# Kernel tuning notes

Hardware: AMD Instinct MI355X
Metric: run time of the kernel (lower is better)

Reference implementation:

```python
import jax, jax.numpy as jnp
import numpy as np

B, H, W, C = 4, 192, 640, 32
S = 32
STEPS = np.arange(S, dtype=np.float32)  # depth steps (init kwarg 'steps')


def setup_inputs() -> dict:
    key = jax.random.key(0)
    k1, k2, k3, k4, k5 = jax.random.split(key, 5)
    x = jax.random.normal(k1, (B, H, W, C), jnp.float32)
    y = jax.random.normal(k2, (B, H, W, C), jnp.float32)
    # principal point near image center, focal ~500px, small translation T12
    origin = jnp.array([[W / 2.0, H / 2.0]], jnp.float32) + jax.random.uniform(k3, (B, 2), jnp.float32)
    focal = 500.0 + 50.0 * jax.random.uniform(k4, (B, 2), jnp.float32)
    T12 = 0.01 * jax.random.normal(k5, (B, 3), jnp.float32)
    return {"x": x, "y": y, "origin": origin, "focal": focal, "T12": T12}


def _bilinear_1img(img, sx, sy):
    # img [H,W,C]; sx [W]: source x-coord for each output column; sy [H]: source y per row.
    # Matches tf.contrib.image.transform BILINEAR with fill value 0 outside the image.
    x0 = jnp.floor(sx); fx = sx - x0
    y0 = jnp.floor(sy); fy = sy - y0
    x0i = x0.astype(jnp.int32); x1i = x0i + 1
    y0i = y0.astype(jnp.int32); y1i = y0i + 1
    mx0 = ((x0i >= 0) & (x0i < W)).astype(img.dtype)
    mx1 = ((x1i >= 0) & (x1i < W)).astype(img.dtype)
    my0 = ((y0i >= 0) & (y0i < H)).astype(img.dtype)
    my1 = ((y1i >= 0) & (y1i < H)).astype(img.dtype)
    # interpolate along y first (transform is separable: x'=a*x+b, y'=a*y+c)
    r0 = img[jnp.clip(y0i, 0, H - 1)]                     # [H,W,C]
    r1 = img[jnp.clip(y1i, 0, H - 1)]                     # [H,W,C]
    rows = (my0 * (1.0 - fy))[:, None, None] * r0 + (my1 * fy)[:, None, None] * r1
    c0 = rows[:, jnp.clip(x0i, 0, W - 1)]                 # [H,W,C]
    c1 = rows[:, jnp.clip(x1i, 0, W - 1)]
    return (mx0 * (1.0 - fx))[None, :, None] * c0 + (mx1 * fx)[None, :, None] * c1


_warp = jax.vmap(lambda img, a, b, c: _bilinear_1img(
    img,
    a * jnp.arange(W, dtype=img.dtype) + b,
    a * jnp.arange(H, dtype=img.dtype) + c))


def reference(x, y, origin, focal, T12):
    tz = T12[:, 2]  # [B]

    def per_step(d):
        safe_d = jnp.where(d == 0.0, 1.0, d)
        D = jnp.where(d == 0.0, 0.0, 1.0 / (1.0 / safe_d + tz))          # [B]
        alpha = 1.0 - D * tz                                              # [B]
        beta = D * tz * origin[:, 0] + D * focal[:, 0] * T12[:, 0]        # [B]
        gamma = D * tz * origin[:, 1] + D * focal[:, 1] * T12[:, 1]       # [B]
        shifted = _warp(x, alpha, beta, gamma)                            # [B,H,W,C]
        return jnp.mean(shifted * y, axis=3)                              # [B,H,W]

    corr = jax.lax.map(jax.checkpoint(per_step), jnp.asarray(STEPS))      # [S,B,H,W]
    return jnp.transpose(corr, (1, 2, 3, 0))                              # [B,H,W,S]
```

## Files before the change

### kernel.cpp

```cpp
#include <hip/hip_runtime.h>
#include <hip/hip_fp16.h>

#define BB 4
#define HH 192
#define WW 640
#define CC 32
#define SS 32
#define PXB 64
#define SPH 8

typedef _Float16 half2n __attribute__((ext_vector_type(2)));

#if defined(__has_builtin)
#if __has_builtin(__builtin_amdgcn_fdot2)
#define HAS_FDOT2 1
#endif
#endif

__global__ __launch_bounds__(256) void convert_x_kernel(const float* __restrict__ x,
                                                        __half* __restrict__ xh) {
    const size_t i = ((size_t)blockIdx.x * 256 + threadIdx.x) * 8;
    const float4 f0 = *(const float4*)(x + i);
    const float4 f1 = *(const float4*)(x + i + 4);
    uint4 u;
    u.x = __builtin_bit_cast(unsigned, __floats2half2_rn(f0.x, f0.y));
    u.y = __builtin_bit_cast(unsigned, __floats2half2_rn(f0.z, f0.w));
    u.z = __builtin_bit_cast(unsigned, __floats2half2_rn(f1.x, f1.y));
    u.w = __builtin_bit_cast(unsigned, __floats2half2_rn(f1.z, f1.w));
    *(uint4*)(xh + i) = u;
}

__global__ __launch_bounds__(256, 7) void corr_kernel(
    const __half* __restrict__ xh, const float* __restrict__ y,
    const float* __restrict__ origin, const float* __restrict__ focal,
    const float* __restrict__ T12, float* __restrict__ out)
{
    __shared__ uint4 sOff[SPH * PXB];
    __shared__ uint4 sWt [SPH * PXB];

    const int tid  = threadIdx.x;
    const int lane = tid & 63;
    const int wave = tid >> 6;
    const int slot = lane >> 2;
    const int cg   = lane & 3;

    const int p0 = blockIdx.x * PXB;
    const int w0 = p0 % WW;
    const int h  = (p0 / WW) % HH;
    const int b  = p0 / (WW * HH);

    const float tz = T12[b * 3 + 2];
    const float kx = tz * origin[b * 2 + 0] + focal[b * 2 + 0] * T12[b * 3 + 0];
    const float ky = tz * origin[b * 2 + 1] + focal[b * 2 + 1] * T12[b * 3 + 1];

    const int pme = p0 + wave * 16 + slot;
    __half2 yh[4];
    {
        const float4 ya = *(const float4*)(y + (size_t)pme * CC + cg * 8);
        const float4 yb = *(const float4*)(y + (size_t)pme * CC + cg * 8 + 4);
        yh[0] = __floats2half2_rn(ya.x, ya.y);
        yh[1] = __floats2half2_rn(ya.z, ya.w);
        yh[2] = __floats2half2_rn(yb.x, yb.y);
        yh[3] = __floats2half2_rn(yb.z, yb.w);
    }

    const char* xbase = (const char*)(xh + (size_t)b * HH * WW * CC);
    const int cgb = cg * 16;
    const int sp  = wave * 16 + slot;

    const int e_px = tid & 63;
    const int e_s0 = tid >> 6;
    const float ewf = (float)(w0 + e_px);
    const float ehf = (float)h;

    float* outp = out + (size_t)pme * SS;

#pragma unroll 1
    for (int ph = 0; ph < 4; ++ph) {
        __syncthreads();
#pragma unroll
        for (int k = 0; k < 2; ++k) {
            const int s_loc = e_s0 + k * 4;
            const int s = ph * SPH + s_loc;
            const float sf = (float)s;
            const float D = sf * __builtin_amdgcn_rcpf(1.0f + sf * tz);
            const float alpha = 1.0f - D * tz;
            const float sx = alpha * ewf + D * kx;
            const float sy = alpha * ehf + D * ky;

            const float x0f = floorf(sx);
            const float y0f = floorf(sy);
            const float fx = sx - x0f;
            const float fy = sy - y0f;
            const int x0 = (int)x0f;
            const int y0 = (int)y0f;
            const int x1 = x0 + 1;
            const int y1 = y0 + 1;

            const float wx0 = (x0 >= 0 && x0 < WW) ? (1.0f - fx) : 0.0f;
            const float wx1 = (x1 >= 0 && x1 < WW) ? fx : 0.0f;
            const float wy0 = (y0 >= 0 && y0 < HH) ? (1.0f - fy) : 0.0f;
            const float wy1 = (y1 >= 0 && y1 < HH) ? fy : 0.0f;

            const int cx0 = min(max(x0, 0), WW - 1);
            const int cx1 = min(max(x1, 0), WW - 1);
            const int cy0 = min(max(y0, 0), HH - 1);
            const int cy1 = min(max(y1, 0), HH - 1);

            const int r0 = cy0 * WW;
            const int r1 = cy1 * WW;
            const uint4 offs = make_uint4((unsigned)((r0 + cx0) << 6),
                                          (unsigned)((r0 + cx1) << 6),
                                          (unsigned)((r1 + cx0) << 6),
                                          (unsigned)((r1 + cx1) << 6));
            auto pk = [](float wgt) -> unsigned {
                const unsigned short us =
                    __builtin_bit_cast(unsigned short, __float2half_rn(wgt));
                return (unsigned)us * 0x10001u;
            };
            const uint4 wts = make_uint4(pk(wy0 * wx0), pk(wy0 * wx1),
                                         pk(wy1 * wx0), pk(wy1 * wx1));
            sOff[s_loc * PXB + e_px] = offs;
            sWt [s_loc * PXB + e_px] = wts;
        }
        __syncthreads();

        float res0 = 0.0f, res1 = 0.0f;

        uint4 o  = sOff[sp];
        uint4 wt = sWt [sp];
        uint4 ua = *(const uint4*)(xbase + (size_t)(o.x + cgb));
        uint4 ub = *(const uint4*)(xbase + (size_t)(o.y + cgb));
        uint4 uc = *(const uint4*)(xbase + (size_t)(o.z + cgb));
        uint4 ud = *(const uint4*)(xbase + (size_t)(o.w + cgb));

#pragma unroll
        for (int j = 0; j < SPH; ++j) {
            uint4 o2, wt2, na, nb, nc, nd;
            if (j + 1 < SPH) {
                o2  = sOff[(j + 1) * PXB + sp];
                wt2 = sWt [(j + 1) * PXB + sp];
                na = *(const uint4*)(xbase + (size_t)(o2.x + cgb));
                nb = *(const uint4*)(xbase + (size_t)(o2.y + cgb));
                nc = *(const uint4*)(xbase + (size_t)(o2.z + cgb));
                nd = *(const uint4*)(xbase + (size_t)(o2.w + cgb));
            }

            const __half2 w00 = __builtin_bit_cast(__half2, wt.x);
            const __half2 w01 = __builtin_bit_cast(__half2, wt.y);
            const __half2 w10 = __builtin_bit_cast(__half2, wt.z);
            const __half2 w11 = __builtin_bit_cast(__half2, wt.w);

            float acc = 0.0f;
#pragma unroll
            for (int i = 0; i < 4; ++i) {
                const unsigned va = (&ua.x)[i];
                const unsigned vb = (&ub.x)[i];
                const unsigned vc = (&uc.x)[i];
                const unsigned vd = (&ud.x)[i];
                __half2 comb = __hmul2(__builtin_bit_cast(__half2, va), w00);
                comb = __hfma2(__builtin_bit_cast(__half2, vb), w01, comb);
                comb = __hfma2(__builtin_bit_cast(__half2, vc), w10, comb);
                comb = __hfma2(__builtin_bit_cast(__half2, vd), w11, comb);
#ifdef HAS_FDOT2
                acc = __builtin_amdgcn_fdot2(__builtin_bit_cast(half2n, comb),
                                             __builtin_bit_cast(half2n, yh[i]),
                                             acc, false);
#else
                const float2 cf = __half22float2(comb);
                const float2 yf = __half22float2(yh[i]);
                acc += cf.x * yf.x + cf.y * yf.y;
#endif
            }

            acc += __shfl_xor(acc, 1, 64);
            acc += __shfl_xor(acc, 2, 64);

            if ((j & 3) == cg) {
                if (j < 4) res0 = acc * (1.0f / 32.0f);
                else       res1 = acc * (1.0f / 32.0f);
            }

            if (j + 1 < SPH) {
                o = o2; wt = wt2; ua = na; ub = nb; uc = nc; ud = nd;
            }
        }
        outp[ph * SPH + cg]     = res0;
        outp[ph * SPH + 4 + cg] = res1;
    }
}

extern "C" void kernel_launch(void* const* d_in, const int* in_sizes, int n_in,
                              void* d_out, int out_size, void* d_ws, size_t ws_size,
                              hipStream_t stream) {
    const float* x = (const float*)d_in[0];
    const float* y = (const float*)d_in[1];
    const float* origin = (const float*)d_in[2];
    const float* focal = (const float*)d_in[3];
    const float* T12 = (const float*)d_in[4];
    float* out = (float*)d_out;
    __half* xh = (__half*)d_ws;

    const int nelem = BB * HH * WW * CC;
    convert_x_kernel<<<nelem / (256 * 8), 256, 0, stream>>>(x, xh);

    const int npix = BB * HH * WW;
    corr_kernel<<<npix / PXB, 256, 0, stream>>>(xh, y, origin, focal, T12, out);
}
```

Baseline: 304.3 us.

## Stage y-interpolated source row segment in LDS per depth step

Exploits the separable warp: since every pixel in a block shares a row and a depth step, the block first y-interpolates the needed source column span of x into double-buffered LDS. Each thread then performs only x-interpolation and the dot product from LDS. This cuts redundant global gathers, which previously fetched four corners per pixel per step. The cost is a __syncthreads per depth step across 32 serialized steps, a fallback path when the span exceeds MAXW, and a change in launch occupancy to 8.

```diff
diff --git a/kernel.cpp b/kernel.cpp
--- a/kernel.cpp
+++ b/kernel.cpp
@@ -7,7 +7,7 @@
 #define CC 32
 #define SS 32
 #define PXB 64
-#define SPH 8
+#define MAXW 152
 
 typedef _Float16 half2n __attribute__((ext_vector_type(2)));
 
@@ -16,6 +16,21 @@
 #define HAS_FDOT2 1
 #endif
 #endif
+
+__device__ __forceinline__ float fdot2_acc(__half2 a, __half2 b, float acc) {
+#ifdef HAS_FDOT2
+    return __builtin_amdgcn_fdot2(__builtin_bit_cast(half2n, a),
+                                  __builtin_bit_cast(half2n, b), acc, false);
+#else
+    const float2 af = __half22float2(a);
+    const float2 bf = __half22float2(b);
+    return acc + af.x * bf.x + af.y * bf.y;
+#endif
+}
+
+__device__ __forceinline__ unsigned pk2(float w) {
+    return (unsigned)__builtin_bit_cast(unsigned short, __float2half_rn(w)) * 0x10001u;
+}
 
 __global__ __launch_bounds__(256) void convert_x_kernel(const float* __restrict__ x,
                                                         __half* __restrict__ xh) {
@@ -30,13 +45,14 @@
     *(uint4*)(xh + i) = u;
 }
 
-__global__ __launch_bounds__(256, 7) void corr_kernel(
+__global__ __launch_bounds__(256, 8) void corr_kernel(
     const __half* __restrict__ xh, const float* __restrict__ y,
     const float* __restrict__ origin, const float* __restrict__ focal,
     const float* __restrict__ T12, float* __restrict__ out)
 {
-    __shared__ uint4 sOff[SPH * PXB];
-    __shared__ uint4 sWt [SPH * PXB];
+    __shared__ uint4 sU[SS];
+    __shared__ uint4 sV[SS];
+    __shared__ uint4 sComb[2][MAXW * 4];
 
     const int tid  = threadIdx.x;
     const int lane = tid & 63;
@@ -49,9 +65,44 @@
     const int h  = (p0 / WW) % HH;
     const int b  = p0 / (WW * HH);
 
-    const float tz = T12[b * 3 + 2];
-    const float kx = tz * origin[b * 2 + 0] + focal[b * 2 + 0] * T12[b * 3 + 0];
-    const float ky = tz * origin[b * 2 + 1] + focal[b * 2 + 1] * T12[b * 3 + 1];
+    if (tid < SS) {
+        const float tz = T12[b * 3 + 2];
+        const float kx = tz * origin[b * 2 + 0] + focal[b * 2 + 0] * T12[b * 3 + 0];
+        const float ky = tz * origin[b * 2 + 1] + focal[b * 2 + 1] * T12[b * 3 + 1];
+        const float sf = (float)tid;
+        const float D = sf * __builtin_amdgcn_rcpf(1.0f + sf * tz);
+        const float alpha = 1.0f - D * tz;
+        const float dkx = D * kx;
+        const float dky = D * ky;
+
+        const float syv = alpha * (float)h + dky;
+        const float y0f = floorf(syv);
+        const float fy  = syv - y0f;
+        const int   y0  = (int)y0f;
+        const int   y1  = y0 + 1;
+        const float wy0 = (y0 >= 0 && y0 < HH) ? (1.0f - fy) : 0.0f;
+        const float wy1 = (y1 >= 0 && y1 < HH) ? fy : 0.0f;
+        const int   cy0 = min(max(y0, 0), HH - 1);
+        const int   cy1 = min(max(y1, 0), HH - 1);
+
+        const float sxa = alpha * (float)w0 + dkx;
+        const float sxb = alpha * (float)(w0 + PXB - 1) + dkx;
+        const int xlo = (int)floorf(fminf(sxa, sxb));
+        const int xhi = (int)floorf(fmaxf(sxa, sxb)) + 1;
+        const int width4 = (xhi - xlo + 1) * 4;
+
+        uint4 U, V;
+        U.x = __builtin_bit_cast(unsigned, alpha);
+        U.y = __builtin_bit_cast(unsigned, dkx);
+        U.z = (unsigned)xlo;
+        U.w = (unsigned)width4;
+        V.x = (unsigned)((cy0 * WW) << 6);
+        V.y = (unsigned)((cy1 * WW) << 6);
+        V.z = pk2(wy0);
+        V.w = pk2(wy1);
+        sU[tid] = U;
+        sV[tid] = V;
+    }
 
     const int pme = p0 + wave * 16 + slot;
     __half2 yh[4];
@@ -66,127 +117,89 @@
 
     const char* xbase = (const char*)(xh + (size_t)b * HH * WW * CC);
     const int cgb = cg * 16;
-    const int sp  = wave * 16 + slot;
-
-    const int e_px = tid & 63;
-    const int e_s0 = tid >> 6;
-    const float ewf = (float)(w0 + e_px);
-    const float ehf = (float)h;
-
+    const float pxf = (float)(w0 + wave * 16 + slot);
     float* outp = out + (size_t)pme * SS;
 
+    __syncthreads();
+
 #pragma unroll 1
-    for (int ph = 0; ph < 4; ++ph) {
-        __syncthreads();
+    for (int s = 0; s < SS; ++s) {
+        const uint4 U = sU[s];
+        const uint4 V = sV[s];
+        const float alpha  = __builtin_bit_cast(float, U.x);
+        const float dkx    = __builtin_bit_cast(float, U.y);
+        const int   xlo    = (int)U.z;
+        const int   width4 = (int)U.w;
+        const int   buf    = s & 1;
+        const bool  fits   = (width4 <= MAXW * 4);
+
+        if (fits) {
+            const __half2 wy0h = __builtin_bit_cast(__half2, V.z);
+            const __half2 wy1h = __builtin_bit_cast(__half2, V.w);
+            for (int c = tid; c < width4; c += 256) {
+                const int cpx = min(max(xlo + (c >> 2), 0), WW - 1);
+                const unsigned po = (unsigned)((cpx << 6) + ((c & 3) << 4));
+                const uint4 a  = *(const uint4*)(xbase + (size_t)(V.x + po));
+                const uint4 bq = *(const uint4*)(xbase + (size_t)(V.y + po));
+                uint4 o;
 #pragma unroll
-        for (int k = 0; k < 2; ++k) {
-            const int s_loc = e_s0 + k * 4;
-            const int s = ph * SPH + s_loc;
-            const float sf = (float)s;
-            const float D = sf * __builtin_amdgcn_rcpf(1.0f + sf * tz);
-            const float alpha = 1.0f - D * tz;
-            const float sx = alpha * ewf + D * kx;
-            const float sy = alpha * ehf + D * ky;
-
-            const float x0f = floorf(sx);
-            const float y0f = floorf(sy);
-            const float fx = sx - x0f;
-            const float fy = sy - y0f;
-            const int x0 = (int)x0f;
-            const int y0 = (int)y0f;
-            const int x1 = x0 + 1;
-            const int y1 = y0 + 1;
-
-            const float wx0 = (x0 >= 0 && x0 < WW) ? (1.0f - fx) : 0.0f;
-            const float wx1 = (x1 >= 0 && x1 < WW) ? fx : 0.0f;
-            const float wy0 = (y0 >= 0 && y0 < HH) ? (1.0f - fy) : 0.0f;
-            const float wy1 = (y1 >= 0 && y1 < HH) ? fy : 0.0f;
-
-            const int cx0 = min(max(x0, 0), WW - 1);
-            const int cx1 = min(max(x1, 0), WW - 1);
-            const int cy0 = min(max(y0, 0), HH - 1);
-            const int cy1 = min(max(y1, 0), HH - 1);
-
-            const int r0 = cy0 * WW;
-            const int r1 = cy1 * WW;
-            const uint4 offs = make_uint4((unsigned)((r0 + cx0) << 6),
-                                          (unsigned)((r0 + cx1) << 6),
-                                          (unsigned)((r1 + cx0) << 6),
-                                          (unsigned)((r1 + cx1) << 6));
-            auto pk = [](float wgt) -> unsigned {
-                const unsigned short us =
-                    __builtin_bit_cast(unsigned short, __float2half_rn(wgt));
-                return (unsigned)us * 0x10001u;
-            };
-            const uint4 wts = make_uint4(pk(wy0 * wx0), pk(wy0 * wx1),
-                                         pk(wy1 * wx0), pk(wy1 * wx1));
-            sOff[s_loc * PXB + e_px] = offs;
-            sWt [s_loc * PXB + e_px] = wts;
+                for (int i = 0; i < 4; ++i) {
+                    __half2 r = __hmul2(__builtin_bit_cast(__half2, (&a.x)[i]), wy0h);
+                    r = __hfma2(__builtin_bit_cast(__half2, (&bq.x)[i]), wy1h, r);
+                    (&o.x)[i] = __builtin_bit_cast(unsigned, r);
+                }
+                sComb[buf][c] = o;
+            }
         }
         __syncthreads();
 
-        float res0 = 0.0f, res1 = 0.0f;
-
-        uint4 o  = sOff[sp];
-        uint4 wt = sWt [sp];
-        uint4 ua = *(const uint4*)(xbase + (size_t)(o.x + cgb));
-        uint4 ub = *(const uint4*)(xbase + (size_t)(o.y + cgb));
-        uint4 uc = *(const uint4*)(xbase + (size_t)(o.z + cgb));
-        uint4 ud = *(const uint4*)(xbase + (size_t)(o.w + cgb));
-
-#pragma unroll
-        for (int j = 0; j < SPH; ++j) {
-            uint4 o2, wt2, na, nb, nc, nd;
-            if (j + 1 < SPH) {
-                o2  = sOff[(j + 1) * PXB + sp];
-                wt2 = sWt [(j + 1) * PXB + sp];
-                na = *(const uint4*)(xbase + (size_t)(o2.x + cgb));
-                nb = *(const uint4*)(xbase + (size_t)(o2.y + cgb));
-                nc = *(const uint4*)(xbase + (size_t)(o2.z + cgb));
-                nd = *(const uint4*)(xbase + (size_t)(o2.w + cgb));
-            }
-
-            const __half2 w00 = __builtin_bit_cast(__half2, wt.x);
-            const __half2 w01 = __builtin_bit_cast(__half2, wt.y);
-            const __half2 w10 = __builtin_bit_cast(__half2, wt.z);
-            const __half2 w11 = __builtin_bit_cast(__half2, wt.w);
-
-            float acc = 0.0f;
+        const float sx  = alpha * pxf + dkx;
+        const float x0f = floorf(sx);
+        const float fx  = sx - x0f;
+        const int   x0  = (int)x0f;
+        const int   x1  = x0 + 1;
+        const float wx0f = (x0 >= 0 && x0 < WW) ? (1.0f - fx) : 0.0f;
+        const float wx1f = (x1 >= 0 && x1 < WW) ? fx : 0.0f;
+        const __half2 wx0 = __builtin_bit_cast(__half2, pk2(wx0f));
+        const __half2 wx1 = __builtin_bit_cast(__half2, pk2(wx1f));
+        const int cx0 = min(max(x0, 0), WW - 1);
+        const int cx1 = min(max(x1, 0), WW - 1);
+
+        float acc = 0.0f;
+        if (fits) {
+            const int wlim = (width4 >> 2) - 1;
+            const int l0 = min(max(cx0 - xlo, 0), wlim);
+            const int l1 = min(max(cx1 - xlo, 0), wlim);
+            const uint4 ca = sComb[buf][l0 * 4 + cg];
+            const uint4 cb = sComb[buf][l1 * 4 + cg];
 #pragma unroll
             for (int i = 0; i < 4; ++i) {
-                const unsigned va = (&ua.x)[i];
-                const unsigned vb = (&ub.x)[i];
-                const unsigned vc = (&uc.x)[i];
-                const unsigned vd = (&ud.x)[i];
-                __half2 comb = __hmul2(__builtin_bit_cast(__half2, va), w00);
-                comb = __hfma2(__builtin_bit_cast(__half2, vb), w01, comb);
-                comb = __hfma2(__builtin_bit_cast(__half2, vc), w10, comb);
-                comb = __hfma2(__builtin_bit_cast(__half2, vd), w11, comb);
-#ifdef HAS_FDOT2
-                acc = __builtin_amdgcn_fdot2(__builtin_bit_cast(half2n, comb),
-                                             __builtin_bit_cast(half2n, yh[i]),
-                                             acc, false);
-#else
-                const float2 cf = __half22float2(comb);
-                const float2 yf = __half22float2(yh[i]);
-                acc += cf.x * yf.x + cf.y * yf.y;
-#endif
+                __half2 v = __hmul2(__builtin_bit_cast(__half2, (&ca.x)[i]), wx0);
+                v = __hfma2(__builtin_bit_cast(__half2, (&cb.x)[i]), wx1, v);
+                acc = fdot2_acc(v, yh[i], acc);
             }
-
-            acc += __shfl_xor(acc, 1, 64);
-            acc += __shfl_xor(acc, 2, 64);
-
-            if ((j & 3) == cg) {
-                if (j < 4) res0 = acc * (1.0f / 32.0f);
-                else       res1 = acc * (1.0f / 32.0f);
-            }
-
-            if (j + 1 < SPH) {
-                o = o2; wt = wt2; ua = na; ub = nb; uc = nc; ud = nd;
+        } else {
+            const __half2 wy0h = __builtin_bit_cast(__half2, V.z);
+            const __half2 wy1h = __builtin_bit_cast(__half2, V.w);
+            const uint4 a  = *(const uint4*)(xbase + (size_t)(V.x + (unsigned)((cx0 << 6) + cgb)));
+            const uint4 bq = *(const uint4*)(xbase + (size_t)(V.x + (unsigned)((cx1 << 6) + cgb)));
+            const uint4 c2 = *(const uint4*)(xbase + (size_t)(V.y + (unsigned)((cx0 << 6) + cgb)));
+            const uint4 d  = *(const uint4*)(xbase + (size_t)(V.y + (unsigned)((cx1 << 6) + cgb)));
+#pragma unroll
+            for (int i = 0; i < 4; ++i) {
+                __half2 top = __hmul2(__builtin_bit_cast(__half2, (&a.x)[i]), wx0);
+                top = __hfma2(__builtin_bit_cast(__half2, (&bq.x)[i]), wx1, top);
+                __half2 bot = __hmul2(__builtin_bit_cast(__half2, (&c2.x)[i]), wx0);
+                bot = __hfma2(__builtin_bit_cast(__half2, (&d.x)[i]), wx1, bot);
+                __half2 v = __hmul2(top, wy0h);
+                v = __hfma2(bot, wy1h, v);
+                acc = fdot2_acc(v, yh[i], acc);
             }
         }
-        outp[ph * SPH + cg]     = res0;
-        outp[ph * SPH + 4 + cg] = res1;
+
+        acc += __shfl_xor(acc, 1, 64);
+        acc += __shfl_xor(acc, 2, 64);
+        if ((s & 3) == cg) outp[s] = acc * (1.0f / 32.0f);
     }
 }
 
```

Measured after the change: 395.4 us. +29.9%, slower.
